# Performance work log

Hardware: AMD Instinct MI355X
Metric: run time of the kernel (lower is better)

Reference implementation:

```python
import jax, jax.numpy as jnp
import numpy as np

NG, NPG, NF = 256, 64, 64          # graphs, nodes/graph, features (NPG == NF: x is per-graph [N,N])
HC, NL = 504, 4                     # hidden_channels, num_layers (HC*NL == TRIU)
E_PER = 1024                        # edges per graph
ALPHA = 0.5
EPS = 1e-5
TRIU = NF * (NF - 1) // 2           # 2016 strict-upper-triangle entries
HIDDEN, NCLS = 1024, 2


def _bn(x, g, b):
    # BatchNorm1d in training mode: biased batch statistics
    m = x.mean(0)
    v = x.var(0)
    return (x - m) * jax.lax.rsqrt(v + EPS) * g + b


def _gcn(x, src, dst, W, b):
    n = x.shape[0]
    xw = x @ W
    deg = jax.ops.segment_sum(jnp.ones(src.shape[0], x.dtype), dst, num_segments=n) + 1.0
    dinv = jax.lax.rsqrt(deg)
    coef = (dinv[src] * dinv[dst])[:, None]
    agg = jax.ops.segment_sum(xw[src] * coef, dst, num_segments=n)
    return agg + xw * (dinv * dinv)[:, None] + b


def _pool(x, batch):
    # global_mean_pool; every graph has exactly NPG nodes
    return jax.ops.segment_sum(x, batch, num_segments=NG) / NPG


def setup_inputs():
    key = jax.random.key(0)
    ks = jax.random.split(key, 16)
    total = NG * NPG
    x = jax.random.normal(ks[0], (total, NF), jnp.float32)
    offs = (jnp.arange(NG) * NPG)[:, None]
    edge_src = (jax.random.randint(ks[1], (NG, E_PER), 0, NPG) + offs).reshape(-1)
    edge_dst = (jax.random.randint(ks[2], (NG, E_PER), 0, NPG) + offs).reshape(-1)
    batch = jnp.arange(total) // NPG

    def lin(k, fi, fo):
        return jax.random.normal(k, (fi, fo), jnp.float32) / np.sqrt(fi)

    Wg0 = lin(ks[3], NF, HC)
    bg0 = jnp.zeros((HC,), jnp.float32)
    Wg_rest = jax.random.normal(ks[4], (NL - 1, HC, HC), jnp.float32) / np.sqrt(HC)
    bg_rest = jnp.zeros((NL - 1, HC), jnp.float32)
    gx = jnp.ones((TRIU,), jnp.float32); bx = jnp.zeros((TRIU,), jnp.float32)
    gh = jnp.ones((HC * NL,), jnp.float32); bh = jnp.zeros((HC * NL,), jnp.float32)
    Watt = lin(ks[5], TRIU, 1); batt = jnp.zeros((1,), jnp.float32)
    D1 = TRIU + HC * NL  # 4032
    Wm1 = lin(ks[6], D1, HIDDEN); bm1 = jnp.zeros((HIDDEN,), jnp.float32)
    gm1 = jnp.ones((HIDDEN,), jnp.float32); bem1 = jnp.zeros((HIDDEN,), jnp.float32)
    Wm2 = lin(ks[7], HIDDEN, HIDDEN // 2); bm2 = jnp.zeros((HIDDEN // 2,), jnp.float32)
    gm2 = jnp.ones((HIDDEN // 2,), jnp.float32); bem2 = jnp.zeros((HIDDEN // 2,), jnp.float32)
    Wm3 = lin(ks[8], HIDDEN // 2, HIDDEN // 2); bm3 = jnp.zeros((HIDDEN // 2,), jnp.float32)
    gm3 = jnp.ones((HIDDEN // 2,), jnp.float32); bem3 = jnp.zeros((HIDDEN // 2,), jnp.float32)
    Wm4 = lin(ks[9], HIDDEN // 2, NCLS); bm4 = jnp.zeros((NCLS,), jnp.float32)
    return dict(x=x, Wg0=Wg0, bg0=bg0, Wg_rest=Wg_rest, bg_rest=bg_rest, gx=gx, bx=bx,
                gh=gh, bh=bh, Watt=Watt, batt=batt, Wm1=Wm1, bm1=bm1, gm1=gm1, bem1=bem1,
                Wm2=Wm2, bm2=bm2, gm2=gm2, bem2=bem2, Wm3=Wm3, bm3=bm3, gm3=gm3, bem3=bem3,
                Wm4=Wm4, bm4=bm4, edge_src=edge_src, edge_dst=edge_dst, batch=batch)


def reference(x, Wg0, bg0, Wg_rest, bg_rest, gx, bx, gh, bh, Watt, batt,
              Wm1, bm1, gm1, bem1, Wm2, bm2, gm2, bem2, Wm3, bm3, gm3, bem3,
              Wm4, bm4, edge_src, edge_dst, batch):
    # stacked GCN convs (no nonlinearity between convs, as in source)
    cur = _gcn(x, edge_src, edge_dst, Wg0, bg0)
    hs = [_pool(cur, batch)]
    for i in range(NL - 1):
        cur = _gcn(cur, edge_src, edge_dst, Wg_rest[i], bg_rest[i])
        hs.append(_pool(cur, batch))
    h = _bn(jnp.concatenate(hs, axis=1), gh, bh)          # [NG, HC*NL]
    # per-graph strict upper triangle of the [N,N] input matrix (== triu().nonzero() trick)
    iu, ju = jnp.triu_indices(NF, k=1)
    xv = x.reshape(NG, NPG, NF)[:, iu, ju]                # [NG, TRIU]
    xv = _bn(xv, gx, bx)
    att = jax.nn.sigmoid(xv @ Watt + batt)                # [NG, 1]
    xf = att * xv + (1.0 - att) * h * ALPHA               # attention-weighted fusion
    z = jnp.concatenate([xf, h], axis=1)                  # [NG, TRIU + HC*NL]
    z = jax.nn.relu(_bn(z @ Wm1 + bm1, gm1, bem1))
    z = jax.nn.relu(_bn(z @ Wm2 + bm2, gm2, bem2))
    z = jax.nn.relu(_bn(z @ Wm3 + bm3, gm3, bem3))
    return z @ Wm4 + bm4                                   # [NG, NCLS]
```

## Files before the change

### kernel.cpp

```cpp
#include <hip/hip_runtime.h>
#include <math.h>

#define NGRAPH 256
#define NPG 64
#define NFEAT 64
#define HC 504
#define NLAY 4
#define EPER 1024
#define NTRIU 2016
#define DCAT 4032
#define HID1 1024
#define HID2 512

#define GCN_LDS (65536 + 73728 + 18432)
#define AHL_LO 4608

typedef __attribute__((ext_vector_type(8))) short bfrag8;
typedef __attribute__((ext_vector_type(4))) float f32x4;

struct __align__(8) us4 { unsigned short a, b, c, d; };

__device__ __forceinline__ unsigned short f2b(float f) {
    union { float f; unsigned u; } v; v.f = f;
    unsigned r = (v.u + 0x7fffu + ((v.u >> 16) & 1u)) >> 16;
    return (unsigned short)r;
}
__device__ __forceinline__ float b2f(unsigned short h) {
    union { unsigned u; float f; } v; v.u = ((unsigned)h) << 16;
    return v.f;
}

__global__ void conv_gcn(const float* __restrict__ Wg0, const float* __restrict__ WgR,
                         unsigned short* __restrict__ Wt0, unsigned short* __restrict__ Wt123)
{
    const int z = blockIdx.z;
    const float* W;
    unsigned short* W4;
    int K, KL;
    if (z == 0) {
        if (blockIdx.y >= 2) return;
        W = Wg0; W4 = Wt0; K = 64; KL = 64;
    } else {
        W = WgR + (size_t)(z - 1) * HC * HC;
        W4 = Wt123 + (size_t)(z - 1) * 262144;
        K = HC; KL = 512;
    }
    __shared__ float T[32][33];
    int k0 = blockIdx.y * 32, n0 = blockIdx.x * 32;
    int tx = threadIdx.x, ty = threadIdx.y;
#pragma unroll
    for (int j = 0; j < 32; j += 8) {
        int k = k0 + ty + j, n = n0 + tx;
        T[ty + j][tx] = (k < K && n < HC) ? W[(size_t)k * HC + n] : 0.f;
    }
    __syncthreads();
#pragma unroll
    for (int j = 0; j < 32; j += 8) {
        int n = n0 + ty + j, k = k0 + tx;
        int idx = ((n >> 4) * (KL >> 5) + (k >> 5)) * 512
                + (((k >> 3) & 3) << 7) + ((n & 15) << 3) + (k & 7);
        W4[idx] = f2b(T[tx][ty + j]);
    }
}

__global__ void conv_mlp(const float* __restrict__ Wm1, const float* __restrict__ Wm2,
                         const float* __restrict__ Wm3,
                         unsigned short* __restrict__ W1t, unsigned short* __restrict__ W2t,
                         unsigned short* __restrict__ W3t)
{
    const int z = blockIdx.z;
    const float* W;
    unsigned short* Wt;
    int K, N;
    if (z == 0)      { W = Wm1; Wt = W1t; K = DCAT; N = HID1; }
    else if (z == 1) { W = Wm2; Wt = W2t; K = HID1; N = HID2; }
    else             { W = Wm3; Wt = W3t; K = HID2; N = HID2; }
    int k0 = blockIdx.y * 32, n0 = blockIdx.x * 32;
    if (k0 >= K || n0 >= N) return;
    __shared__ float T[32][33];
    int tx = threadIdx.x, ty = threadIdx.y;
#pragma unroll
    for (int j = 0; j < 32; j += 8) {
        int k = k0 + ty + j, n = n0 + tx;
        T[ty + j][tx] = (k < K && n < N) ? W[(size_t)k * N + n] : 0.f;
    }
    __syncthreads();
#pragma unroll
    for (int j = 0; j < 32; j += 8) {
        int n = n0 + ty + j, k = k0 + tx;
        Wt[(size_t)n * K + k] = f2b(T[tx][ty + j]);
    }
}

template<int KL>
__device__ __forceinline__ void gcn_layer(const unsigned short* __restrict__ W4,
                                          const float* __restrict__ bias,
                                          unsigned short* cur, unsigned short* xwt,
                                          const unsigned short* ahl,
                                          float* __restrict__ hsg,
                                          int wv, int lm, int lh)
{
    constexpr int KTS = KL >> 5;
    const int colw = wv << 5;
    const int kswz = (lm & 7) << 3;
    const int lane8 = ((lh << 4) + lm) << 3;

    f32x4 acc[4][2];
#pragma unroll
    for (int m0 = 0; m0 < 4; ++m0)
#pragma unroll
        for (int cc = 0; cc < 2; ++cc) acc[m0][cc] = (f32x4){0.f, 0.f, 0.f, 0.f};

    bfrag8 bq[2][2];
#pragma unroll
    for (int cc = 0; cc < 2; ++cc)
        bq[0][cc] = *(const bfrag8*)(const void*)&W4[(size_t)((wv * 2 + cc) * KTS + 0) * 512 + lane8];
    if (KTS > 1) {
#pragma unroll
        for (int cc = 0; cc < 2; ++cc)
            bq[1][cc] = *(const bfrag8*)(const void*)&W4[(size_t)((wv * 2 + cc) * KTS + 1) * 512 + lane8];
    }
#pragma unroll
    for (int kt = 0; kt < KTS; ++kt) {
        bfrag8 a[4];
#pragma unroll
        for (int m0 = 0; m0 < 4; ++m0)
            a[m0] = *(const bfrag8*)(const void*)&cur[(m0 * 16 + lm) * 512 + ((kt * 32 + (lh << 3)) ^ kswz)];
        bfrag8 bc[2];
        bc[0] = bq[kt & 1][0]; bc[1] = bq[kt & 1][1];
        if (kt + 2 < KTS) {
#pragma unroll
            for (int cc = 0; cc < 2; ++cc)
                bq[kt & 1][cc] = *(const bfrag8*)(const void*)&W4[(size_t)((wv * 2 + cc) * KTS + kt + 2) * 512 + lane8];
        }
#pragma unroll
        for (int cc = 0; cc < 2; ++cc)
#pragma unroll
            for (int m0 = 0; m0 < 4; ++m0)
                acc[m0][cc] = __builtin_amdgcn_mfma_f32_16x16x32_bf16(a[m0], bc[cc], acc[m0][cc], 0, 0, 0);
    }
    __syncthreads();

#pragma unroll
    for (int cc = 0; cc < 2; ++cc) {
        const int c = colw + cc * 16 + lm;
#pragma unroll
        for (int m0 = 0; m0 < 4; ++m0) {
            us4 p;
            p.a = f2b(acc[m0][cc][0]); p.b = f2b(acc[m0][cc][1]);
            p.c = f2b(acc[m0][cc][2]); p.d = f2b(acc[m0][cc][3]);
            *(us4*)(void*)&xwt[c * 72 + m0 * 16 + (lh << 2)] = p;
        }
    }

    f32x4 acc2[2][4];
#pragma unroll
    for (int cc = 0; cc < 2; ++cc)
#pragma unroll
        for (int n0 = 0; n0 < 4; ++n0) acc2[cc][n0] = (f32x4){0.f, 0.f, 0.f, 0.f};
#pragma unroll
    for (int n0 = 0; n0 < 4; ++n0) {
        const int o = (n0 * 16 + lm) * 72 + (lh << 3);
        bfrag8 bh0 = *(const bfrag8*)(const void*)&ahl[o];
        bfrag8 bh1 = *(const bfrag8*)(const void*)&ahl[o + 32];
        bfrag8 bl0 = *(const bfrag8*)(const void*)&ahl[AHL_LO + o];
        bfrag8 bl1 = *(const bfrag8*)(const void*)&ahl[AHL_LO + o + 32];
#pragma unroll
        for (int cc = 0; cc < 2; ++cc) {
            const int c = colw + cc * 16 + lm;
            bfrag8 a0 = *(const bfrag8*)(const void*)&xwt[c * 72 + (lh << 3)];
            bfrag8 a1 = *(const bfrag8*)(const void*)&xwt[c * 72 + 32 + (lh << 3)];
            acc2[cc][n0] = __builtin_amdgcn_mfma_f32_16x16x32_bf16(a0, bh0, acc2[cc][n0], 0, 0, 0);
            acc2[cc][n0] = __builtin_amdgcn_mfma_f32_16x16x32_bf16(a0, bl0, acc2[cc][n0], 0, 0, 0);
            acc2[cc][n0] = __builtin_amdgcn_mfma_f32_16x16x32_bf16(a1, bh1, acc2[cc][n0], 0, 0, 0);
            acc2[cc][n0] = __builtin_amdgcn_mfma_f32_16x16x32_bf16(a1, bl1, acc2[cc][n0], 0, 0, 0);
        }
    }

#pragma unroll
    for (int cc = 0; cc < 2; ++cc) {
        const int cb = colw + cc * 16 + (lh << 2);
        float bv[4];
#pragma unroll
        for (int r = 0; r < 4; ++r) {
            int c = cb + r;
            bv[r] = (c < HC) ? bias[c] : 0.f;
        }
        float t0 = 0.f, t1 = 0.f, t2 = 0.f, t3 = 0.f;
#pragma unroll
        for (int n0 = 0; n0 < 4; ++n0) {
            const int d = n0 * 16 + lm;
            float v0 = acc2[cc][n0][0] + bv[0];
            float v1 = acc2[cc][n0][1] + bv[1];
            float v2 = acc2[cc][n0][2] + bv[2];
            float v3 = acc2[cc][n0][3] + bv[3];
            t0 += v0; t1 += v1; t2 += v2; t3 += v3;
            us4 p;
            p.a = f2b(v0); p.b = f2b(v1); p.c = f2b(v2); p.d = f2b(v3);
            *(us4*)(void*)&cur[d * 512 + (cb ^ ((d & 7) << 3))] = p;
        }
#pragma unroll
        for (int m = 1; m < 16; m <<= 1) {
            t0 += __shfl_xor(t0, m, 64);
            t1 += __shfl_xor(t1, m, 64);
            t2 += __shfl_xor(t2, m, 64);
            t3 += __shfl_xor(t3, m, 64);
        }
        if (lm == 0 && cb < HC)
            *(float4*)&hsg[cb] = make_float4(t0 * (1.0f / 64.0f), t1 * (1.0f / 64.0f),
                                             t2 * (1.0f / 64.0f), t3 * (1.0f / 64.0f));
    }
    __syncthreads();
}

__global__ __launch_bounds__(1024, 4) void gcn_all(const float* __restrict__ x,
                                                   const int* __restrict__ esrc,
                                                   const int* __restrict__ edst,
                                                   const unsigned short* __restrict__ Wt0,
                                                   const unsigned short* __restrict__ Wt123,
                                                   const float* __restrict__ bg0,
                                                   const float* __restrict__ bgR,
                                                   float* __restrict__ hs)
{
    extern __shared__ char lds[];
    unsigned short* cur = (unsigned short*)lds;
    unsigned short* xwt = (unsigned short*)(lds + 65536);
    unsigned short* ahl = (unsigned short*)(lds + 65536 + 73728);
    float* Af   = (float*)(lds + 65536);
    int*   cnt  = (int*)(lds + 65536 + 16384);
    float* dinv = (float*)(lds + 65536 + 16384 + 256);

    const int g = blockIdx.x, tid = threadIdx.x;
    const int wv = tid >> 6, lane = tid & 63;
    const int lm = lane & 15, lh = lane >> 4;

    for (int i = tid; i < 4096; i += 1024) Af[i] = 0.f;
    if (tid < 64) cnt[tid] = 0;
    __syncthreads();
    atomicAdd(&cnt[edst[(size_t)g * EPER + tid] & 63], 1);
    __syncthreads();
    if (tid < 64) dinv[tid] = rsqrtf((float)cnt[tid] + 1.0f);
    __syncthreads();
    {
        int s = esrc[(size_t)g * EPER + tid] & 63;
        int d = edst[(size_t)g * EPER + tid] & 63;
        atomicAdd(&Af[d * 64 + s], dinv[s] * dinv[d]);
    }
    __syncthreads();
    if (tid < 64) Af[tid * 64 + tid] += dinv[tid] * dinv[tid];
    __syncthreads();
    for (int i = tid; i < 4096; i += 1024) {
        float v = Af[i];
        unsigned short h = f2b(v);
        int d = i >> 6, s = i & 63;
        ahl[d * 72 + s] = h;
        ahl[AHL_LO + d * 72 + s] = f2b(v - b2f(h));
    }
    {
        float4 v = ((const float4*)(x + (size_t)g * 4096))[tid];
        int row = (tid * 4) >> 6, col = (tid * 4) & 63;
        unsigned short* p = &cur[row * 512 + (col ^ ((row & 7) << 3))];
        p[0] = f2b(v.x); p[1] = f2b(v.y); p[2] = f2b(v.z); p[3] = f2b(v.w);
    }
    __syncthreads();

    float* hsg = hs + (size_t)g * (HC * NLAY);
    gcn_layer<64>(Wt0, bg0, cur, xwt, ahl, hsg, wv, lm, lh);
    for (int l = 1; l < NLAY; ++l)
        gcn_layer<512>(Wt123 + (size_t)(l - 1) * 262144, bgR + (l - 1) * HC,
                       cur, xwt, ahl, hsg + l * HC, wv, lm, lh);
}

__global__ __launch_bounds__(256) void pre_stats(const float* __restrict__ hs,
                                                 const float* __restrict__ x,
                                                 float* __restrict__ xv,
                                                 float* __restrict__ psh,
                                                 float* __restrict__ pssh,
                                                 float* __restrict__ psx,
                                                 float* __restrict__ pssx)
{
    int t = blockIdx.x * 256 + threadIdx.x;
    if (t >= NTRIU) return;
    int g0 = blockIdx.y * 16;
    if (blockIdx.z == 0) {
        float s = 0.f, ss = 0.f;
        for (int g = g0; g < g0 + 16; ++g) {
            float v = hs[(size_t)g * NTRIU + t];
            s += v; ss += v * v;
        }
        psh [(size_t)blockIdx.y * NTRIU + t] = s;
        pssh[(size_t)blockIdx.y * NTRIU + t] = ss;
    } else {
        int i = (int)(63.5f - sqrtf(63.5f * 63.5f - 2.0f * (float)t));
        while (63 * (i + 1) - (i + 1) * i / 2 <= t) ++i;
        while (63 * i - i * (i - 1) / 2 > t) --i;
        int j = t - (63 * i - i * (i - 1) / 2) + i + 1;
        int o = i * 64 + j;
        float s = 0.f, ss = 0.f;
        for (int g = g0; g < g0 + 16; ++g) {
            float v = x[(size_t)g * 4096 + o];
            xv[(size_t)g * NTRIU + t] = v;
            s += v; ss += v * v;
        }
        psx [(size_t)blockIdx.y * NTRIU + t] = s;
        pssx[(size_t)blockIdx.y * NTRIU + t] = ss;
    }
}

__global__ __launch_bounds__(256) void stats_fin2(const float* __restrict__ psh,
                                                  const float* __restrict__ pssh,
                                                  const float* __restrict__ psx,
                                                  const float* __restrict__ pssx,
                                                  float* __restrict__ hm,
                                                  float* __restrict__ hiv,
                                                  float* __restrict__ xm,
                                                  float* __restrict__ xi)
{
    int f = blockIdx.x * 256 + threadIdx.x;
    if (f >= NTRIU) return;
    const float* ps  = blockIdx.y ? psx  : psh;
    const float* pss = blockIdx.y ? pssx : pssh;
    float* mo = blockIdx.y ? xm : hm;
    float* io = blockIdx.y ? xi : hiv;
    float s = 0.f, ss = 0.f;
    for (int b = 0; b < 16; ++b) {
        s  += ps [(size_t)b * NTRIU + f];
        ss += pss[(size_t)b * NTRIU + f];
    }
    float m = s * (1.0f / NGRAPH);
    mo[f] = m;
    io[f] = rsqrtf(ss * (1.0f / NGRAPH) - m * m + 1e-5f);
}

__global__ __launch_bounds__(256) void attz_fused(const float* __restrict__ xv,
                                                  const float* __restrict__ xm,
                                                  const float* __restrict__ xi,
                                                  const float* __restrict__ gx,
                                                  const float* __restrict__ bx,
                                                  const float* __restrict__ hsrc,
                                                  const float* __restrict__ hm,
                                                  const float* __restrict__ hi,
                                                  const float* __restrict__ gh,
                                                  const float* __restrict__ bh,
                                                  const float* __restrict__ Watt,
                                                  const float* __restrict__ batt,
                                                  unsigned short* __restrict__ zhi,
                                                  unsigned short* __restrict__ zlo)
{
    int g = blockIdx.x;
    __shared__ float xs[NTRIU];
    __shared__ float red[256];
    float s = 0.f;
    for (int t = threadIdx.x; t < NTRIU; t += 256) {
        float v = (xv[(size_t)g * NTRIU + t] - xm[t]) * xi[t] * gx[t] + bx[t];
        xs[t] = v;
        s += v * Watt[t];
    }
    red[threadIdx.x] = s;
    __syncthreads();
    for (int w = 128; w > 0; w >>= 1) {
        if (threadIdx.x < w) red[threadIdx.x] += red[threadIdx.x + w];
        __syncthreads();
    }
    float att = 1.0f / (1.0f + expf(-(red[0] + batt[0])));
    for (int t = threadIdx.x; t < NTRIU; t += 256) {
        float hn = (hsrc[(size_t)g * NTRIU + t] - hm[t]) * hi[t] * gh[t] + bh[t];
        float zf = att * xs[t] + (1.0f - att) * hn * 0.5f;
        unsigned short h0 = f2b(zf);
        zhi[(size_t)g * DCAT + t] = h0;
        zlo[(size_t)g * DCAT + t] = f2b(zf - b2f(h0));
        unsigned short h1 = f2b(hn);
        zhi[(size_t)g * DCAT + NTRIU + t] = h1;
        zlo[(size_t)g * DCAT + NTRIU + t] = f2b(hn - b2f(h1));
    }
}

__global__ __launch_bounds__(256) void gemm_bf_sk(const unsigned short* __restrict__ Ahi,
                                                  const unsigned short* __restrict__ Alo,
                                                  const unsigned short* __restrict__ Bt,
                                                  float* __restrict__ P,
                                                  int N, int K, int chunk)
{
    __shared__ unsigned short Ah[2][2048], Al[2][2048], Bs[2][2048];
    const int tid  = threadIdx.x;
    const int wave = tid >> 6, lane = tid & 63;
    const int row0 = blockIdx.y << 6, col0 = blockIdx.x << 6;
    const int kb = blockIdx.z * chunk;
    const int NT = chunk >> 5;
    const int sr = tid >> 2, sk = (tid & 3) << 3;
    const unsigned short* gAh = Ahi + (size_t)(row0 + sr) * K + kb + sk;
    const unsigned short* gAl = Alo + (size_t)(row0 + sr) * K + kb + sk;
    const unsigned short* gB  = Bt  + (size_t)(col0 + sr) * K + kb + sk;

    int4 rh = *(const int4*)(const void*)gAh;
    int4 rl = *(const int4*)(const void*)gAl;
    int4 rb = *(const int4*)(const void*)gB;
    *(int4*)(void*)&Ah[0][tid << 3] = rh;
    *(int4*)(void*)&Al[0][tid << 3] = rl;
    *(int4*)(void*)&Bs[0][tid << 3] = rb;
    __syncthreads();

    f32x4 acc0 = {0.f, 0.f, 0.f, 0.f};
    f32x4 acc1 = acc0, acc2 = acc0, acc3 = acc0;
    const int aoff = (wave * 16 + (lane & 15)) * 32 + ((lane >> 4) << 3);
    const int boff = (lane & 15) * 32 + ((lane >> 4) << 3);

    for (int t = 0; t < NT; ++t) {
        if (t + 1 < NT) {
            rh = *(const int4*)(const void*)(gAh + (t + 1) * 32);
            rl = *(const int4*)(const void*)(gAl + (t + 1) * 32);
            rb = *(const int4*)(const void*)(gB  + (t + 1) * 32);
        }
        const unsigned short* ah = Ah[t & 1];
        const unsigned short* al = Al[t & 1];
        const unsigned short* bs = Bs[t & 1];
        bfrag8 a  = *(const bfrag8*)(const void*)&ah[aoff];
        bfrag8 a2 = *(const bfrag8*)(const void*)&al[aoff];
        bfrag8 b0 = *(const bfrag8*)(const void*)&bs[boff];
        bfrag8 b1 = *(const bfrag8*)(const void*)&bs[boff + 16 * 32];
        bfrag8 b2 = *(const bfrag8*)(const void*)&bs[boff + 32 * 32];
        bfrag8 b3 = *(const bfrag8*)(const void*)&bs[boff + 48 * 32];
        acc0 = __builtin_amdgcn_mfma_f32_16x16x32_bf16(a,  b0, acc0, 0, 0, 0);
        acc0 = __builtin_amdgcn_mfma_f32_16x16x32_bf16(a2, b0, acc0, 0, 0, 0);
        acc1 = __builtin_amdgcn_mfma_f32_16x16x32_bf16(a,  b1, acc1, 0, 0, 0);
        acc1 = __builtin_amdgcn_mfma_f32_16x16x32_bf16(a2, b1, acc1, 0, 0, 0);
        acc2 = __builtin_amdgcn_mfma_f32_16x16x32_bf16(a,  b2, acc2, 0, 0, 0);
        acc2 = __builtin_amdgcn_mfma_f32_16x16x32_bf16(a2, b2, acc2, 0, 0, 0);
        acc3 = __builtin_amdgcn_mfma_f32_16x16x32_bf16(a,  b3, acc3, 0, 0, 0);
        acc3 = __builtin_amdgcn_mfma_f32_16x16x32_bf16(a2, b3, acc3, 0, 0, 0);
        if (t + 1 < NT) {
            *(int4*)(void*)&Ah[(t + 1) & 1][tid << 3] = rh;
            *(int4*)(void*)&Al[(t + 1) & 1][tid << 3] = rl;
            *(int4*)(void*)&Bs[(t + 1) & 1][tid << 3] = rb;
        }
        __syncthreads();
    }

    float* Pp = P + (size_t)blockIdx.z * NGRAPH * N;
    const int rbase = row0 + wave * 16 + ((lane >> 4) << 2);
    const int cbase = col0 + (lane & 15);
#pragma unroll
    for (int r = 0; r < 4; ++r) {
        int grow = rbase + r;
        Pp[(size_t)grow * N + cbase +  0] = acc0[r];
        Pp[(size_t)grow * N + cbase + 16] = acc1[r];
        Pp[(size_t)grow * N + cbase + 32] = acc2[r];
        Pp[(size_t)grow * N + cbase + 48] = acc3[r];
    }
}

__global__ __launch_bounds__(256) void reduce_stats(const float* __restrict__ P,
                                                    const float* __restrict__ bias,
                                                    float* __restrict__ mf,
                                                    float* __restrict__ ps,
                                                    float* __restrict__ pss,
                                                    int N, int S)
{
    int f = blockIdx.x * 256 + threadIdx.x;
    int r0 = blockIdx.y * 8;
    size_t MN = (size_t)NGRAPH * N;
    float bv = bias[f];
    float s = 0.f, ss = 0.f;
    for (int r = r0; r < r0 + 8; ++r) {
        float v = 0.f;
        for (int t = 0; t < S; ++t) v += P[(size_t)t * MN + (size_t)r * N + f];
        v += bv;
        mf[(size_t)r * N + f] = v;
        s += v; ss += v * v;
    }
    ps [(size_t)blockIdx.y * N + f] = s;
    pss[(size_t)blockIdx.y * N + f] = ss;
}

__global__ __launch_bounds__(256) void fin_apply(const float* __restrict__ ps,
                                                 const float* __restrict__ pss,
                                                 const float* __restrict__ mf,
                                                 const float* __restrict__ gamma,
                                                 const float* __restrict__ beta,
                                                 unsigned short* __restrict__ hi,
                                                 unsigned short* __restrict__ lo,
                                                 int N)
{
    int f = blockIdx.x * 256 + threadIdx.x;
    float s = 0.f, ss = 0.f;
#pragma unroll 8
    for (int b = 0; b < 32; ++b) {
        s  += ps [(size_t)b * N + f];
        ss += pss[(size_t)b * N + f];
    }
    float m  = s * (1.0f / NGRAPH);
    float iv = rsqrtf(ss * (1.0f / NGRAPH) - m * m + 1e-5f) * gamma[f];
    float bt = beta[f];
    int r0 = blockIdx.y * 8;
    for (int r = r0; r < r0 + 8; ++r) {
        float v = (mf[(size_t)r * N + f] - m) * iv + bt;
        v = fmaxf(v, 0.f);
        unsigned short h = f2b(v);
        hi[(size_t)r * N + f] = h;
        lo[(size_t)r * N + f] = f2b(v - b2f(h));
    }
}

__global__ __launch_bounds__(256) void final_kernel(const unsigned short* __restrict__ Xhi,
                                                    const unsigned short* __restrict__ Xlo,
                                                    const float* __restrict__ W,
                                                    const float* __restrict__ b,
                                                    float* __restrict__ out)
{
    int g = blockIdx.x;
    float s0 = 0.f, s1 = 0.f;
    for (int k = threadIdx.x; k < HID2; k += 256) {
        float v = b2f(Xhi[(size_t)g * HID2 + k]) + b2f(Xlo[(size_t)g * HID2 + k]);
        s0 += v * W[k * 2 + 0];
        s1 += v * W[k * 2 + 1];
    }
    __shared__ float r0[256], r1[256];
    r0[threadIdx.x] = s0; r1[threadIdx.x] = s1;
    __syncthreads();
    for (int w = 128; w > 0; w >>= 1) {
        if (threadIdx.x < w) {
            r0[threadIdx.x] += r0[threadIdx.x + w];
            r1[threadIdx.x] += r1[threadIdx.x + w];
        }
        __syncthreads();
    }
    if (threadIdx.x == 0) {
        out[g * 2 + 0] = r0[0] + b[0];
        out[g * 2 + 1] = r1[0] + b[1];
    }
}

extern "C" void kernel_launch(void* const* d_in, const int* in_sizes, int n_in,
                              void* d_out, int out_size, void* d_ws, size_t ws_size,
                              hipStream_t stream)
{
    const float* x      = (const float*)d_in[0];
    const float* Wg0    = (const float*)d_in[1];
    const float* bg0    = (const float*)d_in[2];
    const float* WgR    = (const float*)d_in[3];
    const float* bgR    = (const float*)d_in[4];
    const float* gx     = (const float*)d_in[5];
    const float* bx     = (const float*)d_in[6];
    const float* gh     = (const float*)d_in[7];
    const float* bh     = (const float*)d_in[8];
    const float* Watt   = (const float*)d_in[9];
    const float* batt   = (const float*)d_in[10];
    const float* Wm1    = (const float*)d_in[11];
    const float* bm1    = (const float*)d_in[12];
    const float* gm1    = (const float*)d_in[13];
    const float* bem1   = (const float*)d_in[14];
    const float* Wm2    = (const float*)d_in[15];
    const float* bm2    = (const float*)d_in[16];
    const float* gm2    = (const float*)d_in[17];
    const float* bem2   = (const float*)d_in[18];
    const float* Wm3    = (const float*)d_in[19];
    const float* bm3    = (const float*)d_in[20];
    const float* gm3    = (const float*)d_in[21];
    const float* bem3   = (const float*)d_in[22];
    const float* Wm4    = (const float*)d_in[23];
    const float* bm4    = (const float*)d_in[24];
    const int*   esrc   = (const int*)d_in[25];
    const int*   edst   = (const int*)d_in[26];
    float* out = (float*)d_out;

    char* w = (char*)d_ws;
    auto alloc = [&](size_t bytes) -> char* {
        char* p = w;
        w += (bytes + 255) & ~(size_t)255;
        return p;
    };
    unsigned short* Wt0   = (unsigned short*)alloc((size_t)512 * 64 * 2);
    unsigned short* Wt123 = (unsigned short*)alloc((size_t)3 * 512 * 512 * 2);
    unsigned short* W1t   = (unsigned short*)alloc((size_t)HID1 * DCAT * 2);
    unsigned short* W2t   = (unsigned short*)alloc((size_t)HID2 * HID1 * 2);
    unsigned short* W3t   = (unsigned short*)alloc((size_t)HID2 * HID2 * 2);
    float*          hs    = (float*)alloc((size_t)NGRAPH * NTRIU * 4);
    float*          xv    = (float*)alloc((size_t)NGRAPH * NTRIU * 4);
    unsigned short* zhi   = (unsigned short*)alloc((size_t)NGRAPH * DCAT * 2);
    unsigned short* zlo   = (unsigned short*)alloc((size_t)NGRAPH * DCAT * 2);
    float*          P     = (float*)alloc((size_t)8 * NGRAPH * HID1 * 4);
    float*          mf    = (float*)alloc((size_t)NGRAPH * HID1 * 4);
    unsigned short* m1hi  = (unsigned short*)alloc((size_t)NGRAPH * HID1 * 2);
    unsigned short* m1lo  = (unsigned short*)alloc((size_t)NGRAPH * HID1 * 2);
    unsigned short* m2hi  = (unsigned short*)alloc((size_t)NGRAPH * HID2 * 2);
    unsigned short* m2lo  = (unsigned short*)alloc((size_t)NGRAPH * HID2 * 2);
    unsigned short* m3hi  = (unsigned short*)alloc((size_t)NGRAPH * HID2 * 2);
    unsigned short* m3lo  = (unsigned short*)alloc((size_t)NGRAPH * HID2 * 2);
    float*          psh   = (float*)alloc((size_t)16 * NTRIU * 4);
    float*          pssh  = (float*)alloc((size_t)16 * NTRIU * 4);
    float*          psx   = (float*)alloc((size_t)16 * NTRIU * 4);
    float*          pssx  = (float*)alloc((size_t)16 * NTRIU * 4);
    float*          ps    = (float*)alloc((size_t)32 * HID1 * 4);
    float*          pss   = (float*)alloc((size_t)32 * HID1 * 4);
    float*          xm    = (float*)alloc(NTRIU * 4);
    float*          xi    = (float*)alloc(NTRIU * 4);
    float*          hm    = (float*)alloc(NTRIU * 4);
    float*          hiv   = (float*)alloc(NTRIU * 4);

    hipFuncSetAttribute((const void*)gcn_all,
                        hipFuncAttributeMaxDynamicSharedMemorySize, GCN_LDS);

    conv_gcn<<<dim3(16, 16, 4), dim3(32, 8), 0, stream>>>(Wg0, WgR, Wt0, Wt123);
    conv_mlp<<<dim3(32, 126, 3), dim3(32, 8), 0, stream>>>(Wm1, Wm2, Wm3, W1t, W2t, W3t);

    gcn_all<<<NGRAPH, 1024, GCN_LDS, stream>>>(x, esrc, edst, Wt0, Wt123, bg0, bgR, hs);

    pre_stats<<<dim3(8, 16, 2), 256, 0, stream>>>(hs, x, xv, psh, pssh, psx, pssx);
    stats_fin2<<<dim3(8, 2), 256, 0, stream>>>(psh, pssh, psx, pssx, hm, hiv, xm, xi);
    attz_fused<<<NGRAPH, 256, 0, stream>>>(xv, xm, xi, gx, bx, hs, hm, hiv, gh, bh,
                                           Watt, batt, zhi, zlo);

    gemm_bf_sk<<<dim3(16, 4, 7), 256, 0, stream>>>(zhi, zlo, W1t, P, HID1, DCAT, 576);
    reduce_stats<<<dim3(4, 32), 256, 0, stream>>>(P, bm1, mf, ps, pss, HID1, 7);
    fin_apply<<<dim3(4, 32), 256, 0, stream>>>(ps, pss, mf, gm1, bem1, m1hi, m1lo, HID1);

    gemm_bf_sk<<<dim3(8, 4, 8), 256, 0, stream>>>(m1hi, m1lo, W2t, P, HID2, HID1, 128);
    reduce_stats<<<dim3(2, 32), 256, 0, stream>>>(P, bm2, mf, ps, pss, HID2, 8);
    fin_apply<<<dim3(2, 32), 256, 0, stream>>>(ps, pss, mf, gm2, bem2, m2hi, m2lo, HID2);

    gemm_bf_sk<<<dim3(8, 4, 8), 256, 0, stream>>>(m2hi, m2lo, W3t, P, HID2, HID2, 64);
    reduce_stats<<<dim3(2, 32), 256, 0, stream>>>(P, bm3, mf, ps, pss, HID2, 8);
    fin_apply<<<dim3(2, 32), 256, 0, stream>>>(ps, pss, mf, gm3, bem3, m3hi, m3lo, HID2);

    final_kernel<<<NGRAPH, 256, 0, stream>>>(m3hi, m3lo, Wm4, bm4, out);
}
```

Baseline: 162.2 us.

## Fuse BN finalize/apply into neighbouring kernels and merge weight conversion launches

Merges the two weight-conversion kernels into one launch. BatchNorm statistic finalization moves into the partial-stats kernels through a last-block atomic counter, which removes the separate stats_fin2 and fin_apply launches. BN apply plus ReLU, along with the hi/lo bf16 split, is folded into the A-tile staging of a new GEMM kernel and into the final classifier kernel. The aim is fewer launches and fewer intermediate buffer round-trips, at the cost of a memset for the counters, threadfence and atomic synchronization, and redundant BN math per GEMM tile.

```diff
diff --git a/kernel.cpp b/kernel.cpp
--- a/kernel.cpp
+++ b/kernel.cpp
@@ -30,65 +30,62 @@
     return v.f;
 }
 
-__global__ void conv_gcn(const float* __restrict__ Wg0, const float* __restrict__ WgR,
-                         unsigned short* __restrict__ Wt0, unsigned short* __restrict__ Wt123)
+__global__ void conv_all(const float* __restrict__ Wg0, const float* __restrict__ WgR,
+                         const float* __restrict__ Wm1, const float* __restrict__ Wm2,
+                         const float* __restrict__ Wm3,
+                         unsigned short* __restrict__ Wt0, unsigned short* __restrict__ Wt123,
+                         unsigned short* __restrict__ W1t, unsigned short* __restrict__ W2t,
+                         unsigned short* __restrict__ W3t)
 {
     const int z = blockIdx.z;
-    const float* W;
-    unsigned short* W4;
-    int K, KL;
-    if (z == 0) {
-        if (blockIdx.y >= 2) return;
-        W = Wg0; W4 = Wt0; K = 64; KL = 64;
-    } else {
-        W = WgR + (size_t)(z - 1) * HC * HC;
-        W4 = Wt123 + (size_t)(z - 1) * 262144;
-        K = HC; KL = 512;
-    }
     __shared__ float T[32][33];
     int k0 = blockIdx.y * 32, n0 = blockIdx.x * 32;
     int tx = threadIdx.x, ty = threadIdx.y;
-#pragma unroll
-    for (int j = 0; j < 32; j += 8) {
-        int k = k0 + ty + j, n = n0 + tx;
-        T[ty + j][tx] = (k < K && n < HC) ? W[(size_t)k * HC + n] : 0.f;
-    }
-    __syncthreads();
-#pragma unroll
-    for (int j = 0; j < 32; j += 8) {
-        int n = n0 + ty + j, k = k0 + tx;
-        int idx = ((n >> 4) * (KL >> 5) + (k >> 5)) * 512
-                + (((k >> 3) & 3) << 7) + ((n & 15) << 3) + (k & 7);
-        W4[idx] = f2b(T[tx][ty + j]);
-    }
-}
-
-__global__ void conv_mlp(const float* __restrict__ Wm1, const float* __restrict__ Wm2,
-                         const float* __restrict__ Wm3,
-                         unsigned short* __restrict__ W1t, unsigned short* __restrict__ W2t,
-                         unsigned short* __restrict__ W3t)
-{
-    const int z = blockIdx.z;
-    const float* W;
-    unsigned short* Wt;
-    int K, N;
-    if (z == 0)      { W = Wm1; Wt = W1t; K = DCAT; N = HID1; }
-    else if (z == 1) { W = Wm2; Wt = W2t; K = HID1; N = HID2; }
-    else             { W = Wm3; Wt = W3t; K = HID2; N = HID2; }
-    int k0 = blockIdx.y * 32, n0 = blockIdx.x * 32;
-    if (k0 >= K || n0 >= N) return;
-    __shared__ float T[32][33];
-    int tx = threadIdx.x, ty = threadIdx.y;
-#pragma unroll
-    for (int j = 0; j < 32; j += 8) {
-        int k = k0 + ty + j, n = n0 + tx;
-        T[ty + j][tx] = (k < K && n < N) ? W[(size_t)k * N + n] : 0.f;
-    }
-    __syncthreads();
-#pragma unroll
-    for (int j = 0; j < 32; j += 8) {
-        int n = n0 + ty + j, k = k0 + tx;
-        Wt[(size_t)n * K + k] = f2b(T[tx][ty + j]);
+    if (z < 4) {
+        const float* W;
+        unsigned short* W4;
+        int K, KL;
+        if (z == 0) {
+            if (blockIdx.y >= 2 || blockIdx.x >= 16) return;
+            W = Wg0; W4 = Wt0; K = 64; KL = 64;
+        } else {
+            if (blockIdx.y >= 16 || blockIdx.x >= 16) return;
+            W = WgR + (size_t)(z - 1) * HC * HC;
+            W4 = Wt123 + (size_t)(z - 1) * 262144;
+            K = HC; KL = 512;
+        }
+#pragma unroll
+        for (int j = 0; j < 32; j += 8) {
+            int k = k0 + ty + j, n = n0 + tx;
+            T[ty + j][tx] = (k < K && n < HC) ? W[(size_t)k * HC + n] : 0.f;
+        }
+        __syncthreads();
+#pragma unroll
+        for (int j = 0; j < 32; j += 8) {
+            int n = n0 + ty + j, k = k0 + tx;
+            int idx = ((n >> 4) * (KL >> 5) + (k >> 5)) * 512
+                    + (((k >> 3) & 3) << 7) + ((n & 15) << 3) + (k & 7);
+            W4[idx] = f2b(T[tx][ty + j]);
+        }
+    } else {
+        const float* W;
+        unsigned short* Wt;
+        int K, N;
+        if (z == 4)      { W = Wm1; Wt = W1t; K = DCAT; N = HID1; }
+        else if (z == 5) { W = Wm2; Wt = W2t; K = HID1; N = HID2; }
+        else             { W = Wm3; Wt = W3t; K = HID2; N = HID2; }
+        if (k0 >= K || n0 >= N) return;
+#pragma unroll
+        for (int j = 0; j < 32; j += 8) {
+            int k = k0 + ty + j, n = n0 + tx;
+            T[ty + j][tx] = (k < K && n < N) ? W[(size_t)k * N + n] : 0.f;
+        }
+        __syncthreads();
+#pragma unroll
+        for (int j = 0; j < 32; j += 8) {
+            int n = n0 + ty + j, k = k0 + tx;
+            Wt[(size_t)n * K + k] = f2b(T[tx][ty + j]);
+        }
     }
 }
 
@@ -277,59 +274,61 @@
                                                  float* __restrict__ psh,
                                                  float* __restrict__ pssh,
                                                  float* __restrict__ psx,
-                                                 float* __restrict__ pssx)
-{
-    int t = blockIdx.x * 256 + threadIdx.x;
-    if (t >= NTRIU) return;
-    int g0 = blockIdx.y * 16;
-    if (blockIdx.z == 0) {
-        float s = 0.f, ss = 0.f;
-        for (int g = g0; g < g0 + 16; ++g) {
-            float v = hs[(size_t)g * NTRIU + t];
-            s += v; ss += v * v;
-        }
-        psh [(size_t)blockIdx.y * NTRIU + t] = s;
-        pssh[(size_t)blockIdx.y * NTRIU + t] = ss;
-    } else {
-        int i = (int)(63.5f - sqrtf(63.5f * 63.5f - 2.0f * (float)t));
-        while (63 * (i + 1) - (i + 1) * i / 2 <= t) ++i;
-        while (63 * i - i * (i - 1) / 2 > t) --i;
-        int j = t - (63 * i - i * (i - 1) / 2) + i + 1;
-        int o = i * 64 + j;
-        float s = 0.f, ss = 0.f;
-        for (int g = g0; g < g0 + 16; ++g) {
-            float v = x[(size_t)g * 4096 + o];
-            xv[(size_t)g * NTRIU + t] = v;
-            s += v; ss += v * v;
-        }
-        psx [(size_t)blockIdx.y * NTRIU + t] = s;
-        pssx[(size_t)blockIdx.y * NTRIU + t] = ss;
-    }
-}
-
-__global__ __launch_bounds__(256) void stats_fin2(const float* __restrict__ psh,
-                                                  const float* __restrict__ pssh,
-                                                  const float* __restrict__ psx,
-                                                  const float* __restrict__ pssx,
-                                                  float* __restrict__ hm,
-                                                  float* __restrict__ hiv,
-                                                  float* __restrict__ xm,
-                                                  float* __restrict__ xi)
-{
-    int f = blockIdx.x * 256 + threadIdx.x;
-    if (f >= NTRIU) return;
-    const float* ps  = blockIdx.y ? psx  : psh;
-    const float* pss = blockIdx.y ? pssx : pssh;
-    float* mo = blockIdx.y ? xm : hm;
-    float* io = blockIdx.y ? xi : hiv;
-    float s = 0.f, ss = 0.f;
-    for (int b = 0; b < 16; ++b) {
-        s  += ps [(size_t)b * NTRIU + f];
-        ss += pss[(size_t)b * NTRIU + f];
-    }
-    float m = s * (1.0f / NGRAPH);
-    mo[f] = m;
-    io[f] = rsqrtf(ss * (1.0f / NGRAPH) - m * m + 1e-5f);
+                                                 float* __restrict__ pssx,
+                                                 float* __restrict__ hm,
+                                                 float* __restrict__ hiv,
+                                                 float* __restrict__ xm,
+                                                 float* __restrict__ xi,
+                                                 int* __restrict__ cnt)
+{
+    const int xj = blockIdx.x, yj = blockIdx.y, zj = blockIdx.z;
+    const int t = xj * 256 + threadIdx.x;
+    if (t < NTRIU) {
+        int g0 = yj * 16;
+        if (zj == 0) {
+            float s = 0.f, ss = 0.f;
+            for (int g = g0; g < g0 + 16; ++g) {
+                float v = hs[(size_t)g * NTRIU + t];
+                s += v; ss += v * v;
+            }
+            psh [(size_t)yj * NTRIU + t] = s;
+            pssh[(size_t)yj * NTRIU + t] = ss;
+        } else {
+            int i = (int)(63.5f - sqrtf(63.5f * 63.5f - 2.0f * (float)t));
+            while (63 * (i + 1) - (i + 1) * i / 2 <= t) ++i;
+            while (63 * i - i * (i - 1) / 2 > t) --i;
+            int j = t - (63 * i - i * (i - 1) / 2) + i + 1;
+            int o = i * 64 + j;
+            float s = 0.f, ss = 0.f;
+            for (int g = g0; g < g0 + 16; ++g) {
+                float v = x[(size_t)g * 4096 + o];
+                xv[(size_t)g * NTRIU + t] = v;
+                s += v; ss += v * v;
+            }
+            psx [(size_t)yj * NTRIU + t] = s;
+            pssx[(size_t)yj * NTRIU + t] = ss;
+        }
+    }
+    __threadfence();
+    __shared__ int last;
+    if (threadIdx.x == 0)
+        last = (atomicAdd(&cnt[zj * 8 + xj], 1) == 15);
+    __syncthreads();
+    if (last) {
+        __threadfence();
+        if (t < NTRIU) {
+            const float* ps  = zj ? psx  : psh;
+            const float* pss = zj ? pssx : pssh;
+            float s = 0.f, ss = 0.f;
+            for (int b = 0; b < 16; ++b) {
+                s  += ps [(size_t)b * NTRIU + t];
+                ss += pss[(size_t)b * NTRIU + t];
+            }
+            float m = s * (1.0f / NGRAPH);
+            if (zj) { xm[t] = m; xi[t]  = rsqrtf(ss * (1.0f / NGRAPH) - m * m + 1e-5f); }
+            else    { hm[t] = m; hiv[t] = rsqrtf(ss * (1.0f / NGRAPH) - m * m + 1e-5f); }
+        }
+    }
 }
 
 __global__ __launch_bounds__(256) void attz_fused(const float* __restrict__ xv,
@@ -449,15 +448,122 @@
     }
 }
 
+__global__ __launch_bounds__(256) void gemm_bn_sk(const float* __restrict__ Af,
+                                                  const float* __restrict__ mean,
+                                                  const float* __restrict__ inv,
+                                                  const float* __restrict__ gamma,
+                                                  const float* __restrict__ beta,
+                                                  const unsigned short* __restrict__ Bt,
+                                                  float* __restrict__ P,
+                                                  int N, int K, int chunk)
+{
+    __shared__ unsigned short Ah[2][2048], Al[2][2048], Bs[2][2048];
+    const int tid  = threadIdx.x;
+    const int wave = tid >> 6, lane = tid & 63;
+    const int row0 = blockIdx.y << 6, col0 = blockIdx.x << 6;
+    const int kb = blockIdx.z * chunk;
+    const int NT = chunk >> 5;
+    const int sr = tid >> 2, sk = (tid & 3) << 3;
+    const float* gA = Af + (size_t)(row0 + sr) * K + kb + sk;
+    const unsigned short* gB = Bt + (size_t)(col0 + sr) * K + kb + sk;
+
+    float4 xa, xb;
+    int4 rb;
+
+    auto stage_a = [&](int buf, float4 v0, float4 v1, int t) {
+        int ks = kb + t * 32 + sk;
+        float4 m0 = *(const float4*)&mean[ks],  m1 = *(const float4*)&mean[ks + 4];
+        float4 i0 = *(const float4*)&inv[ks],   i1 = *(const float4*)&inv[ks + 4];
+        float4 g0 = *(const float4*)&gamma[ks], g1 = *(const float4*)&gamma[ks + 4];
+        float4 b0 = *(const float4*)&beta[ks],  b1 = *(const float4*)&beta[ks + 4];
+        float v[8] = {v0.x, v0.y, v0.z, v0.w, v1.x, v1.y, v1.z, v1.w};
+        float m[8] = {m0.x, m0.y, m0.z, m0.w, m1.x, m1.y, m1.z, m1.w};
+        float iv[8] = {i0.x, i0.y, i0.z, i0.w, i1.x, i1.y, i1.z, i1.w};
+        float ga[8] = {g0.x, g0.y, g0.z, g0.w, g1.x, g1.y, g1.z, g1.w};
+        float be[8] = {b0.x, b0.y, b0.z, b0.w, b1.x, b1.y, b1.z, b1.w};
+        unsigned short h[8], l[8];
+#pragma unroll
+        for (int q = 0; q < 8; ++q) {
+            float w = fmaxf((v[q] - m[q]) * iv[q] * ga[q] + be[q], 0.f);
+            h[q] = f2b(w);
+            l[q] = f2b(w - b2f(h[q]));
+        }
+        us4 ph0 = {h[0], h[1], h[2], h[3]}, ph1 = {h[4], h[5], h[6], h[7]};
+        us4 pl0 = {l[0], l[1], l[2], l[3]}, pl1 = {l[4], l[5], l[6], l[7]};
+        *(us4*)(void*)&Ah[buf][tid << 3]       = ph0;
+        *(us4*)(void*)&Ah[buf][(tid << 3) + 4] = ph1;
+        *(us4*)(void*)&Al[buf][tid << 3]       = pl0;
+        *(us4*)(void*)&Al[buf][(tid << 3) + 4] = pl1;
+    };
+
+    xa = *(const float4*)gA;
+    xb = *(const float4*)(gA + 4);
+    rb = *(const int4*)(const void*)gB;
+    stage_a(0, xa, xb, 0);
+    *(int4*)(void*)&Bs[0][tid << 3] = rb;
+    __syncthreads();
+
+    f32x4 acc0 = {0.f, 0.f, 0.f, 0.f};
+    f32x4 acc1 = acc0, acc2 = acc0, acc3 = acc0;
+    const int aoff = (wave * 16 + (lane & 15)) * 32 + ((lane >> 4) << 3);
+    const int boff = (lane & 15) * 32 + ((lane >> 4) << 3);
+
+    for (int t = 0; t < NT; ++t) {
+        if (t + 1 < NT) {
+            xa = *(const float4*)(gA + (t + 1) * 32);
+            xb = *(const float4*)(gA + (t + 1) * 32 + 4);
+            rb = *(const int4*)(const void*)(gB + (t + 1) * 32);
+        }
+        const unsigned short* ah = Ah[t & 1];
+        const unsigned short* al = Al[t & 1];
+        const unsigned short* bs = Bs[t & 1];
+        bfrag8 a  = *(const bfrag8*)(const void*)&ah[aoff];
+        bfrag8 a2 = *(const bfrag8*)(const void*)&al[aoff];
+        bfrag8 b0 = *(const bfrag8*)(const void*)&bs[boff];
+        bfrag8 b1 = *(const bfrag8*)(const void*)&bs[boff + 16 * 32];
+        bfrag8 b2 = *(const bfrag8*)(const void*)&bs[boff + 32 * 32];
+        bfrag8 b3 = *(const bfrag8*)(const void*)&bs[boff + 48 * 32];
+        acc0 = __builtin_amdgcn_mfma_f32_16x16x32_bf16(a,  b0, acc0, 0, 0, 0);
+        acc0 = __builtin_amdgcn_mfma_f32_16x16x32_bf16(a2, b0, acc0, 0, 0, 0);
+        acc1 = __builtin_amdgcn_mfma_f32_16x16x32_bf16(a,  b1, acc1, 0, 0, 0);
+        acc1 = __builtin_amdgcn_mfma_f32_16x16x32_bf16(a2, b1, acc1, 0, 0, 0);
+        acc2 = __builtin_amdgcn_mfma_f32_16x16x32_bf16(a,  b2, acc2, 0, 0, 0);
+        acc2 = __builtin_amdgcn_mfma_f32_16x16x32_bf16(a2, b2, acc2, 0, 0, 0);
+        acc3 = __builtin_amdgcn_mfma_f32_16x16x32_bf16(a,  b3, acc3, 0, 0, 0);
+        acc3 = __builtin_amdgcn_mfma_f32_16x16x32_bf16(a2, b3, acc3, 0, 0, 0);
+        if (t + 1 < NT) {
+            stage_a((t + 1) & 1, xa, xb, t + 1);
+            *(int4*)(void*)&Bs[(t + 1) & 1][tid << 3] = rb;
+        }
+        __syncthreads();
+    }
+
+    float* Pp = P + (size_t)blockIdx.z * NGRAPH * N;
+    const int rbase = row0 + wave * 16 + ((lane >> 4) << 2);
+    const int cbase = col0 + (lane & 15);
+#pragma unroll
+    for (int r = 0; r < 4; ++r) {
+        int grow = rbase + r;
+        Pp[(size_t)grow * N + cbase +  0] = acc0[r];
+        Pp[(size_t)grow * N + cbase + 16] = acc1[r];
+        Pp[(size_t)grow * N + cbase + 32] = acc2[r];
+        Pp[(size_t)grow * N + cbase + 48] = acc3[r];
+    }
+}
+
 __global__ __launch_bounds__(256) void reduce_stats(const float* __restrict__ P,
                                                     const float* __restrict__ bias,
                                                     float* __restrict__ mf,
                                                     float* __restrict__ ps,
                                                     float* __restrict__ pss,
-                                                    int N, int S)
-{
-    int f = blockIdx.x * 256 + threadIdx.x;
-    int r0 = blockIdx.y * 8;
+                                                    float* __restrict__ mean,
+                                                    float* __restrict__ inv,
+                                                    int N, int S,
+                                                    int* __restrict__ cnt, int slotBase)
+{
+    const int xj = blockIdx.x, yj = blockIdx.y;
+    int f = xj * 256 + threadIdx.x;
+    int r0 = yj * 8;
     size_t MN = (size_t)NGRAPH * N;
     float bv = bias[f];
     float s = 0.f, ss = 0.f;
@@ -468,49 +574,39 @@
         mf[(size_t)r * N + f] = v;
         s += v; ss += v * v;
     }
-    ps [(size_t)blockIdx.y * N + f] = s;
-    pss[(size_t)blockIdx.y * N + f] = ss;
-}
-
-__global__ __launch_bounds__(256) void fin_apply(const float* __restrict__ ps,
-                                                 const float* __restrict__ pss,
-                                                 const float* __restrict__ mf,
-                                                 const float* __restrict__ gamma,
-                                                 const float* __restrict__ beta,
-                                                 unsigned short* __restrict__ hi,
-                                                 unsigned short* __restrict__ lo,
-                                                 int N)
-{
-    int f = blockIdx.x * 256 + threadIdx.x;
-    float s = 0.f, ss = 0.f;
-#pragma unroll 8
-    for (int b = 0; b < 32; ++b) {
-        s  += ps [(size_t)b * N + f];
-        ss += pss[(size_t)b * N + f];
-    }
-    float m  = s * (1.0f / NGRAPH);
-    float iv = rsqrtf(ss * (1.0f / NGRAPH) - m * m + 1e-5f) * gamma[f];
-    float bt = beta[f];
-    int r0 = blockIdx.y * 8;
-    for (int r = r0; r < r0 + 8; ++r) {
-        float v = (mf[(size_t)r * N + f] - m) * iv + bt;
-        v = fmaxf(v, 0.f);
-        unsigned short h = f2b(v);
-        hi[(size_t)r * N + f] = h;
-        lo[(size_t)r * N + f] = f2b(v - b2f(h));
-    }
-}
-
-__global__ __launch_bounds__(256) void final_kernel(const unsigned short* __restrict__ Xhi,
-                                                    const unsigned short* __restrict__ Xlo,
-                                                    const float* __restrict__ W,
-                                                    const float* __restrict__ b,
-                                                    float* __restrict__ out)
+    ps [(size_t)yj * N + f] = s;
+    pss[(size_t)yj * N + f] = ss;
+    __threadfence();
+    __shared__ int last;
+    if (threadIdx.x == 0)
+        last = (atomicAdd(&cnt[slotBase + xj], 1) == 31);
+    __syncthreads();
+    if (last) {
+        __threadfence();
+        float S1 = 0.f, S2 = 0.f;
+        for (int b = 0; b < 32; ++b) {
+            S1 += ps [(size_t)b * N + f];
+            S2 += pss[(size_t)b * N + f];
+        }
+        float m = S1 * (1.0f / NGRAPH);
+        mean[f] = m;
+        inv[f]  = rsqrtf(S2 * (1.0f / NGRAPH) - m * m + 1e-5f);
+    }
+}
+
+__global__ __launch_bounds__(256) void final_bn(const float* __restrict__ mf,
+                                                const float* __restrict__ mean,
+                                                const float* __restrict__ inv,
+                                                const float* __restrict__ gamma,
+                                                const float* __restrict__ beta,
+                                                const float* __restrict__ W,
+                                                const float* __restrict__ b,
+                                                float* __restrict__ out)
 {
     int g = blockIdx.x;
     float s0 = 0.f, s1 = 0.f;
     for (int k = threadIdx.x; k < HID2; k += 256) {
-        float v = b2f(Xhi[(size_t)g * HID2 + k]) + b2f(Xlo[(size_t)g * HID2 + k]);
+        float v = fmaxf((mf[(size_t)g * HID2 + k] - mean[k]) * inv[k] * gamma[k] + beta[k], 0.f);
         s0 += v * W[k * 2 + 0];
         s1 += v * W[k * 2 + 1];
     }
@@ -580,12 +676,6 @@
     unsigned short* zlo   = (unsigned short*)alloc((size_t)NGRAPH * DCAT * 2);
     float*          P     = (float*)alloc((size_t)8 * NGRAPH * HID1 * 4);
     float*          mf    = (float*)alloc((size_t)NGRAPH * HID1 * 4);
-    unsigned short* m1hi  = (unsigned short*)alloc((size_t)NGRAPH * HID1 * 2);
-    unsigned short* m1lo  = (unsigned short*)alloc((size_t)NGRAPH * HID1 * 2);
-    unsigned short* m2hi  = (unsigned short*)alloc((size_t)NGRAPH * HID2 * 2);
-    unsigned short* m2lo  = (unsigned short*)alloc((size_t)NGRAPH * HID2 * 2);
-    unsigned short* m3hi  = (unsigned short*)alloc((size_t)NGRAPH * HID2 * 2);
-    unsigned short* m3lo  = (unsigned short*)alloc((size_t)NGRAPH * HID2 * 2);
     float*          psh   = (float*)alloc((size_t)16 * NTRIU * 4);
     float*          pssh  = (float*)alloc((size_t)16 * NTRIU * 4);
     float*          psx   = (float*)alloc((size_t)16 * NTRIU * 4);
@@ -596,31 +686,38 @@
     float*          xi    = (float*)alloc(NTRIU * 4);
     float*          hm    = (float*)alloc(NTRIU * 4);
     float*          hiv   = (float*)alloc(NTRIU * 4);
+    float*          mmean = (float*)alloc(HID1 * 4);
+    float*          minv  = (float*)alloc(HID1 * 4);
+    int*            cnt   = (int*)alloc(128);
 
     hipFuncSetAttribute((const void*)gcn_all,
                         hipFuncAttributeMaxDynamicSharedMemorySize, GCN_LDS);
 
-    conv_gcn<<<dim3(16, 16, 4), dim3(32, 8), 0, stream>>>(Wg0, WgR, Wt0, Wt123);
-    conv_mlp<<<dim3(32, 126, 3), dim3(32, 8), 0, stream>>>(Wm1, Wm2, Wm3, W1t, W2t, W3t);
+    hipMemsetAsync(cnt, 0, 128, stream);
+
+    conv_all<<<dim3(32, 126, 7), dim3(32, 8), 0, stream>>>(Wg0, WgR, Wm1, Wm2, Wm3,
+                                                           Wt0, Wt123, W1t, W2t, W3t);
 
     gcn_all<<<NGRAPH, 1024, GCN_LDS, stream>>>(x, esrc, edst, Wt0, Wt123, bg0, bgR, hs);
 
-    pre_stats<<<dim3(8, 16, 2), 256, 0, stream>>>(hs, x, xv, psh, pssh, psx, pssx);
-    stats_fin2<<<dim3(8, 2), 256, 0, stream>>>(psh, pssh, psx, pssx, hm, hiv, xm, xi);
+    pre_stats<<<dim3(8, 16, 2), 256, 0, stream>>>(hs, x, xv, psh, pssh, psx, pssx,
+                                                  hm, hiv, xm, xi, cnt);
     attz_fused<<<NGRAPH, 256, 0, stream>>>(xv, xm, xi, gx, bx, hs, hm, hiv, gh, bh,
                                            Watt, batt, zhi, zlo);
 
     gemm_bf_sk<<<dim3(16, 4, 7), 256, 0, stream>>>(zhi, zlo, W1t, P, HID1, DCAT, 576);
-    reduce_stats<<<dim3(4, 32), 256, 0, stream>>>(P, bm1, mf, ps, pss, HID1, 7);
-    fin_apply<<<dim3(4, 32), 256, 0, stream>>>(ps, pss, mf, gm1, bem1, m1hi, m1lo, HID1);
-
-    gemm_bf_sk<<<dim3(8, 4, 8), 256, 0, stream>>>(m1hi, m1lo, W2t, P, HID2, HID1, 128);
-    reduce_stats<<<dim3(2, 32), 256, 0, stream>>>(P, bm2, mf, ps, pss, HID2, 8);
-    fin_apply<<<dim3(2, 32), 256, 0, stream>>>(ps, pss, mf, gm2, bem2, m2hi, m2lo, HID2);
-
-    gemm_bf_sk<<<dim3(8, 4, 8), 256, 0, stream>>>(m2hi, m2lo, W3t, P, HID2, HID2, 64);
-    reduce_stats<<<dim3(2, 32), 256, 0, stream>>>(P, bm3, mf, ps, pss, HID2, 8);
-    fin_apply<<<dim3(2, 32), 256, 0, stream>>>(ps, pss, mf, gm3, bem3, m3hi, m3lo, HID2);
-
-    final_kernel<<<NGRAPH, 256, 0, stream>>>(m3hi, m3lo, Wm4, bm4, out);
-}
+    reduce_stats<<<dim3(4, 32), 256, 0, stream>>>(P, bm1, mf, ps, pss, mmean, minv,
+                                                  HID1, 7, cnt, 16);
+
+    gemm_bn_sk<<<dim3(8, 4, 8), 256, 0, stream>>>(mf, mmean, minv, gm1, bem1, W2t, P,
+                                                  HID2, HID1, 128);
+    reduce_stats<<<dim3(2, 32), 256, 0, stream>>>(P, bm2, mf, ps, pss, mmean, minv,
+                                                  HID2, 8, cnt, 20);
+
+    gemm_bn_sk<<<dim3(8, 4, 8), 256, 0, stream>>>(mf, mmean, minv, gm2, bem2, W3t, P,
+                                                  HID2, HID2, 64);
+    reduce_stats<<<dim3(2, 32), 256, 0, stream>>>(P, bm3, mf, ps, pss, mmean, minv,
+                                                  HID2, 8, cnt, 22);
+
+    final_bn<<<NGRAPH, 256, 0, stream>>>(mf, mmean, minv, gm3, bem3, Wm4, bm4, out);
+}
```

After: 203.1 us. +25.2%, slower.
